# Kernel tuning notes

Measured on AMD Instinct MI355X. Metric: run time of the kernel, lower is better.

Reference implementation:

```python
import jax, jax.numpy as jnp
import numpy as np

B, C, CO, H, W = 64, 64, 64, 56, 56
E, K = 8, 2


def _conv3x3(x, k, b):
    # x: [B,C,H,W], k: [CO,C,3,3], b: [CO]
    y = jax.lax.conv_general_dilated(
        x, k, window_strides=(1, 1), padding='SAME',
        dimension_numbers=('NCHW', 'OIHW', 'NCHW'))
    return y + b[None, :, None, None]


def setup_inputs() -> dict:
    key = jax.random.key(0)
    k1, k2, k3, k4, k5 = jax.random.split(key, 5)
    x = jax.random.normal(k1, (B, C, H, W), dtype=jnp.float32)
    weights = jax.random.uniform(k2, (B, K), dtype=jnp.float32)
    indices = jax.random.randint(k3, (B, K), 0, E, dtype=jnp.int32)
    W_exp = jax.random.normal(k4, (E, CO, C, 3, 3), dtype=jnp.float32) * 0.05
    b_exp = jax.random.normal(k5, (E, CO), dtype=jnp.float32) * 0.01
    return {'x': x, 'weights': weights, 'indices': indices,
            'W_exp': W_exp, 'b_exp': b_exp}


def reference(x, weights, indices, W_exp, b_exp):
    # Dense-equivalent MoE dispatch: run every expert on the full batch,
    # then gather the top-k expert outputs per sample and combine.
    # Same math as the masked gather / index_add_ loop in the torch module.
    # acts: [E, B, CO, H, W]
    acts = jax.vmap(lambda k, b: jax.nn.relu(_conv3x3(x, k, b)))(W_exp, b_exp)
    acts_b = jnp.transpose(acts, (1, 0, 2, 3, 4))  # [B, E, CO, H, W]
    idx = indices[:, :, None, None, None].astype(jnp.int32)
    sel = jnp.take_along_axis(acts_b, idx, axis=1)  # [B, K, CO, H, W]
    out = jnp.sum(sel * weights[:, :, None, None, None], axis=1)  # [B, CO, H, W]
    return out
```

## Files before the change

kernel.cpp:

```cpp
#include <hip/hip_runtime.h>


#define BB 64
#define CC 64
#define COO 64
#define HH 56
#define WW 56

typedef __bf16 bf16x8 __attribute__((ext_vector_type(8)));
typedef float  f32x4  __attribute__((ext_vector_type(4)));

__global__ __launch_bounds__(256) void xpose_kernel(
    const float* __restrict__ x, __bf16* __restrict__ xT)
{
    const int b   = blockIdx.y;
    const int hp  = blockIdx.x;
    const int tid = threadIdx.x;
    __shared__ float tile[CC][WW + 1];

    __bf16* dst = xT + ((size_t)b * 58 + hp) * 66 * CC;
    const bool interior = (hp >= 1 && hp <= HH);

    if (!interior) {
        bf16x8 z = {};
        for (int j = tid; j < 66 * CC / 8; j += 256)
            *(bf16x8*)(dst + j * 8) = z;
        return;
    }

    const int h = hp - 1;
    const float* xb = x + (size_t)b * CC * HH * WW + (size_t)h * WW;
    for (int i = tid; i < CC * 14; i += 256) {
        const int c = i / 14, wq = i % 14;
        const float4 f = *(const float4*)(xb + (size_t)c * HH * WW + wq * 4);
        tile[c][wq * 4 + 0] = f.x; tile[c][wq * 4 + 1] = f.y;
        tile[c][wq * 4 + 2] = f.z; tile[c][wq * 4 + 3] = f.w;
    }
    __syncthreads();
    for (int j = tid; j < 66 * 8; j += 256) {
        const int wc = j >> 3, cg = j & 7;
        bf16x8 v = {};
        if (wc >= 1 && wc <= WW) {
            const int w = wc - 1;
            #pragma unroll
            for (int u = 0; u < 8; ++u) v[u] = (__bf16)tile[cg * 8 + u][w];
        }
        *(bf16x8*)(dst + wc * CC + cg * 8) = v;
    }
}

__global__ __launch_bounds__(256) void wpack_kernel(
    const float* __restrict__ Wexp, __bf16* __restrict__ Wpack)
{
    const int rs = blockIdx.x;
    const int e  = blockIdx.y;
    const int r = rs / 3, s = rs % 3;
    for (int idx = threadIdx.x; idx < 4096; idx += 256) {
        const int ks   = idx >> 11;
        const int rem  = idx & 2047;
        const int mt   = rem >> 9;
        const int lane = (rem >> 3) & 63;
        const int j    = idx & 7;
        const int co = mt * 16 + (lane & 15);
        const int c  = ks * 32 + ((lane >> 4) << 3) + j;
        const float v = Wexp[((((size_t)e * COO + co) * CC + c) * 3 + r) * 3 + s];
        Wpack[(size_t)e * 36864 + (size_t)rs * 4096 + idx] = (__bf16)v;
    }
}

__global__ __launch_bounds__(256, 2) void moe_conv_mfma(
    const __bf16* __restrict__ xT, const __bf16* __restrict__ Wpack,
    const float* __restrict__ gate_w, const int* __restrict__ gate_i,
    const float* __restrict__ bexp, float* __restrict__ out)
{
    __shared__ __bf16 ldsA[2 * 12288];

    const int b   = blockIdx.y;
    const int h0  = blockIdx.x * 4;
    const int tid = threadIdx.x;
    const int wid = tid >> 6, lane = tid & 63;
    const int n15 = lane & 15, quad = lane >> 4;
    const int wcol = wid * 16 + n15;

    const int   e0 = gate_i[b * 2 + 0], e1 = gate_i[b * 2 + 1];
    const float g0 = gate_w[b * 2 + 0], g1 = gate_w[b * 2 + 1];

    const __bf16* xb = xT + (size_t)b * 58 * 66 * CC;

    f32x4 acc[2][4][4] = {};

    for (int r = 0; r < 3; ++r) {
        __syncthreads();
        {
            const __bf16* s0 = Wpack + (size_t)e0 * 36864 + r * 12288;
            const __bf16* s1 = Wpack + (size_t)e1 * 36864 + r * 12288;
            #pragma unroll
            for (int i = 0; i < 12; ++i) {
                const int q    = wid * 12 + i;
                const int slot = q >= 24;
                const int rem  = q - slot * 24;
                const __bf16* src = (slot ? s1 : s0) + rem * 512 + lane * 8;
                const uint4 tmp = *(const uint4*)src;
                *(uint4*)&ldsA[q * 512 + lane * 8] = tmp;
            }
        }
        __syncthreads();

        #pragma unroll
        for (int s = 0; s < 3; ++s) {
            #pragma unroll
            for (int ks = 0; ks < 2; ++ks) {
                bf16x8 bf[4];
                #pragma unroll
                for (int t = 0; t < 4; ++t) {
                    const int hr1 = h0 + t + r;
                    const int wc1 = wcol + s;
                    bf[t] = *(const bf16x8*)(
                        xb + (size_t)(hr1 * 66 + wc1) * CC + ks * 32 + quad * 8);
                }
                #pragma unroll
                for (int slot = 0; slot < 2; ++slot) {
                    #pragma unroll
                    for (int mt = 0; mt < 4; ++mt) {
                        const bf16x8 af = *(const bf16x8*)
                            &ldsA[slot * 12288 + (s * 2 + ks) * 2048 + mt * 512 + lane * 8];
                        #pragma unroll
                        for (int t = 0; t < 4; ++t)
                            acc[slot][mt][t] = __builtin_amdgcn_mfma_f32_16x16x32_bf16(
                                af, bf[t], acc[slot][mt][t], 0, 0, 0);
                    }
                }
            }
        }
    }

    if (wcol < WW) {
        #pragma unroll
        for (int t = 0; t < 4; ++t) {
            const int h = h0 + t;
            #pragma unroll
            for (int mt = 0; mt < 4; ++mt) {
                #pragma unroll
                for (int v = 0; v < 4; ++v) {
                    const int co = mt * 16 + quad * 4 + v;
                    float a0 = acc[0][mt][t][v] + bexp[e0 * COO + co];
                    float a1 = acc[1][mt][t][v] + bexp[e1 * COO + co];
                    a0 = fmaxf(a0, 0.f);
                    a1 = fmaxf(a1, 0.f);
                    out[(((size_t)b * COO + co) * HH + h) * WW + wcol] =
                        g0 * a0 + g1 * a1;
                }
            }
        }
    }
}

extern "C" void kernel_launch(void* const* d_in, const int* in_sizes, int n_in,
                              void* d_out, int out_size, void* d_ws, size_t ws_size,
                              hipStream_t stream) {
    const float* x      = (const float*)d_in[0];
    const float* gate_w = (const float*)d_in[1];
    const int*   gate_i = (const int*)  d_in[2];
    const float* Wexp   = (const float*)d_in[3];
    const float* bexp   = (const float*)d_in[4];
    float* out = (float*)d_out;

    __bf16* Wpack = (__bf16*)d_ws;
    __bf16* xT    = (__bf16*)((char*)d_ws + 589824);

    xpose_kernel<<<dim3(58, BB), 256, 0, stream>>>(x, xT);
    wpack_kernel<<<dim3(9, 8),  256, 0, stream>>>(Wexp, Wpack);
    moe_conv_mfma<<<dim3(14, BB), 256, 0, stream>>>(xT, Wpack, gate_w, gate_i,
                                                    bexp, out);
}
```

Measured before the change: 163.5 us.

## Fuse input transpose into conv kernel with swizzled LDS halo tile and register-prefetched weights

Removes the separate transpose kernel and its global bf16 intermediate. Each conv block now loads its 6-row halo of fp32 input directly, converts it to bf16 and stores it in LDS with an XOR swizzle. It reads B fragments from LDS instead of global memory and prefetches the next tap's weight slice into registers while the current tap computes. This saves a launch and a global round trip, but adds redundant halo loads across blocks, more LDS use (about 60KB) and a syncthreads per tap, which may limit occupancy.

```diff
diff --git a/kernel.cpp b/kernel.cpp
--- a/kernel.cpp
+++ b/kernel.cpp
@@ -9,45 +9,6 @@
 
 typedef __bf16 bf16x8 __attribute__((ext_vector_type(8)));
 typedef float  f32x4  __attribute__((ext_vector_type(4)));
-
-__global__ __launch_bounds__(256) void xpose_kernel(
-    const float* __restrict__ x, __bf16* __restrict__ xT)
-{
-    const int b   = blockIdx.y;
-    const int hp  = blockIdx.x;
-    const int tid = threadIdx.x;
-    __shared__ float tile[CC][WW + 1];
-
-    __bf16* dst = xT + ((size_t)b * 58 + hp) * 66 * CC;
-    const bool interior = (hp >= 1 && hp <= HH);
-
-    if (!interior) {
-        bf16x8 z = {};
-        for (int j = tid; j < 66 * CC / 8; j += 256)
-            *(bf16x8*)(dst + j * 8) = z;
-        return;
-    }
-
-    const int h = hp - 1;
-    const float* xb = x + (size_t)b * CC * HH * WW + (size_t)h * WW;
-    for (int i = tid; i < CC * 14; i += 256) {
-        const int c = i / 14, wq = i % 14;
-        const float4 f = *(const float4*)(xb + (size_t)c * HH * WW + wq * 4);
-        tile[c][wq * 4 + 0] = f.x; tile[c][wq * 4 + 1] = f.y;
-        tile[c][wq * 4 + 2] = f.z; tile[c][wq * 4 + 3] = f.w;
-    }
-    __syncthreads();
-    for (int j = tid; j < 66 * 8; j += 256) {
-        const int wc = j >> 3, cg = j & 7;
-        bf16x8 v = {};
-        if (wc >= 1 && wc <= WW) {
-            const int w = wc - 1;
-            #pragma unroll
-            for (int u = 0; u < 8; ++u) v[u] = (__bf16)tile[cg * 8 + u][w];
-        }
-        *(bf16x8*)(dst + wc * CC + cg * 8) = v;
-    }
-}
 
 __global__ __launch_bounds__(256) void wpack_kernel(
     const float* __restrict__ Wexp, __bf16* __restrict__ Wpack)
@@ -68,12 +29,15 @@
     }
 }
 
-__global__ __launch_bounds__(256, 2) void moe_conv_mfma(
-    const __bf16* __restrict__ xT, const __bf16* __restrict__ Wpack,
+__global__ __launch_bounds__(256, 2) void moe_conv_fused(
+    const float* __restrict__ x, const __bf16* __restrict__ Wpack,
     const float* __restrict__ gate_w, const int* __restrict__ gate_i,
     const float* __restrict__ bexp, float* __restrict__ out)
 {
-    __shared__ __bf16 ldsA[2 * 12288];
+    __shared__ __attribute__((aligned(16))) char smem[44544 + 16384];
+    __bf16* Bs   = (__bf16*)smem;
+    float*  scr  = (float*)(smem + 44544);
+    __bf16* ldsA = (__bf16*)(smem + 44544);
 
     const int b   = blockIdx.y;
     const int h0  = blockIdx.x * 4;
@@ -85,50 +49,79 @@
     const int   e0 = gate_i[b * 2 + 0], e1 = gate_i[b * 2 + 1];
     const float g0 = gate_w[b * 2 + 0], g1 = gate_w[b * 2 + 1];
 
-    const __bf16* xb = xT + (size_t)b * 58 * 66 * CC;
+    const __bf16* s0p = Wpack + (size_t)e0 * 36864;
+    const __bf16* s1p = Wpack + (size_t)e1 * 36864;
+
+    uint4 apre[4];
+    #pragma unroll
+    for (int i = 0; i < 4; ++i)
+        apre[i] = *(const uint4*)((i < 2 ? s0p : s1p) + (size_t)((i & 1) * 256 + tid) * 8);
+
+    #pragma unroll 1
+    for (int rr = 0; rr < 6; ++rr) {
+        const int h = h0 + rr - 1;
+        const bool valid = (h >= 0) && (h < HH);
+        if (valid) {
+            for (int i = tid; i < CC * 14; i += 256) {
+                const int c = i / 14, wq = i - c * 14;
+                const float4 f = *(const float4*)(
+                    x + (((size_t)b * CC + c) * HH + h) * WW + wq * 4);
+                float* sp = &scr[c * 57 + wq * 4];
+                sp[0] = f.x; sp[1] = f.y; sp[2] = f.z; sp[3] = f.w;
+            }
+        }
+        __syncthreads();
+        for (int j = tid; j < 58 * 8; j += 256) {
+            const int wc = j >> 3, cg = j & 7;
+            bf16x8 v = {};
+            if (valid && wc >= 1 && wc <= WW) {
+                const int w = wc - 1;
+                #pragma unroll
+                for (int u = 0; u < 8; ++u) v[u] = (__bf16)scr[(cg * 8 + u) * 57 + w];
+            }
+            *(bf16x8*)&Bs[(size_t)(((rr * 58 + wc) * 8) + (cg ^ (wc & 7))) * 8] = v;
+        }
+        __syncthreads();
+    }
 
     f32x4 acc[2][4][4] = {};
 
-    for (int r = 0; r < 3; ++r) {
+    #pragma unroll 1
+    for (int p = 0; p < 9; ++p) {
+        const int r = p / 3, s = p - r * 3;
+
         __syncthreads();
-        {
-            const __bf16* s0 = Wpack + (size_t)e0 * 36864 + r * 12288;
-            const __bf16* s1 = Wpack + (size_t)e1 * 36864 + r * 12288;
+        #pragma unroll
+        for (int i = 0; i < 4; ++i)
+            *(uint4*)&ldsA[(size_t)(i * 256 + tid) * 8] = apre[i];
+        if (p < 8) {
             #pragma unroll
-            for (int i = 0; i < 12; ++i) {
-                const int q    = wid * 12 + i;
-                const int slot = q >= 24;
-                const int rem  = q - slot * 24;
-                const __bf16* src = (slot ? s1 : s0) + rem * 512 + lane * 8;
-                const uint4 tmp = *(const uint4*)src;
-                *(uint4*)&ldsA[q * 512 + lane * 8] = tmp;
-            }
+            for (int i = 0; i < 4; ++i)
+                apre[i] = *(const uint4*)((i < 2 ? s0p : s1p)
+                          + (size_t)(p + 1) * 4096 + (size_t)((i & 1) * 256 + tid) * 8);
         }
         __syncthreads();
 
+        const int wc1 = min(wcol + s, 57);
         #pragma unroll
-        for (int s = 0; s < 3; ++s) {
+        for (int ks = 0; ks < 2; ++ks) {
+            bf16x8 bfr[4];
             #pragma unroll
-            for (int ks = 0; ks < 2; ++ks) {
-                bf16x8 bf[4];
+            for (int t = 0; t < 4; ++t) {
+                const int rr = t + r;
+                const int cb = ((rr * 58 + wc1) * 8) + ((ks * 4 + quad) ^ (wc1 & 7));
+                bfr[t] = *(const bf16x8*)&Bs[(size_t)cb * 8];
+            }
+            #pragma unroll
+            for (int slot = 0; slot < 2; ++slot) {
                 #pragma unroll
-                for (int t = 0; t < 4; ++t) {
-                    const int hr1 = h0 + t + r;
-                    const int wc1 = wcol + s;
-                    bf[t] = *(const bf16x8*)(
-                        xb + (size_t)(hr1 * 66 + wc1) * CC + ks * 32 + quad * 8);
-                }
-                #pragma unroll
-                for (int slot = 0; slot < 2; ++slot) {
+                for (int mt = 0; mt < 4; ++mt) {
+                    const bf16x8 af = *(const bf16x8*)
+                        &ldsA[(size_t)(slot * 4096 + ks * 2048 + mt * 512 + lane * 8)];
                     #pragma unroll
-                    for (int mt = 0; mt < 4; ++mt) {
-                        const bf16x8 af = *(const bf16x8*)
-                            &ldsA[slot * 12288 + (s * 2 + ks) * 2048 + mt * 512 + lane * 8];
-                        #pragma unroll
-                        for (int t = 0; t < 4; ++t)
-                            acc[slot][mt][t] = __builtin_amdgcn_mfma_f32_16x16x32_bf16(
-                                af, bf[t], acc[slot][mt][t], 0, 0, 0);
-                    }
+                    for (int t = 0; t < 4; ++t)
+                        acc[slot][mt][t] = __builtin_amdgcn_mfma_f32_16x16x32_bf16(
+                            af, bfr[t], acc[slot][mt][t], 0, 0, 0);
                 }
             }
         }
@@ -166,10 +159,8 @@
     float* out = (float*)d_out;
 
     __bf16* Wpack = (__bf16*)d_ws;
-    __bf16* xT    = (__bf16*)((char*)d_ws + 589824);
 
-    xpose_kernel<<<dim3(58, BB), 256, 0, stream>>>(x, xT);
-    wpack_kernel<<<dim3(9, 8),  256, 0, stream>>>(Wexp, Wpack);
-    moe_conv_mfma<<<dim3(14, BB), 256, 0, stream>>>(xT, Wpack, gate_w, gate_i,
-                                                    bexp, out);
+    wpack_kernel<<<dim3(9, 8), 256, 0, stream>>>(Wexp, Wpack);
+    moe_conv_fused<<<dim3(14, BB), 256, 0, stream>>>(x, Wpack, gate_w, gate_i,
+                                                     bexp, out);
 }
```

After: 173.9 us. 1.06x slower.
